# Kernel tuning notes

Measured on AMD Instinct MI355X. Metric: run time of the kernel, lower is better.

## Reference

```python
import jax, jax.numpy as jnp
import numpy as np

N_NEIGHBORS = 9
MIN_STD, MAX_STD = 0.01, 0.5
EPS = 1e-8


def setup_inputs() -> dict:
    key = jax.random.key(0)
    k1, k2, k3 = jax.random.split(key, 3)
    B, C, H, W = 8, 2048, 28, 28
    M = 8192
    features = jax.random.normal(k1, (B, C, H, W), dtype=jnp.float32)
    memory_bank = jax.random.normal(k2, (M, C), dtype=jnp.float32)
    influence_weight = jnp.ones((C,), dtype=jnp.float32)
    distance_weight = jnp.ones((1,), dtype=jnp.float32)
    noise_unit = jax.random.normal(k3, (B * H * W, C), dtype=jnp.float32)
    return {
        "features": features,
        "memory_bank": memory_bank,
        "influence_weight": influence_weight,
        "distance_weight": distance_weight,
        "noise_unit": noise_unit,
    }


def _std(x, axis=None, keepdims=False):
    # torch.std default: unbiased (ddof=1)
    return jnp.std(x, axis=axis, keepdims=keepdims, ddof=1)


def reference(features, memory_bank, influence_weight, distance_weight, noise_unit):
    B, C, H, W = features.shape
    M = memory_bank.shape[0]
    k = min(N_NEIGHBORS, M)

    # [B*H*W, C]
    f = features.transpose(0, 2, 3, 1).reshape(B * H * W, C)

    # Euclidean cdist via the (||a||^2 + ||b||^2 - 2 a.b) expansion
    f2 = jnp.sum(f * f, axis=1, keepdims=True)            # [N,1]
    m2 = jnp.sum(memory_bank * memory_bank, axis=1)       # [M]
    d2 = f2 + m2[None, :] - 2.0 * (f @ memory_bank.T)     # [N,M]
    dist = jnp.sqrt(jnp.clip(d2, 0.0, None))

    # top-k smallest distances (sorted ascending, like torch.topk largest=False)
    neg_vals, idx = jax.lax.top_k(-dist, k)               # [N,k]
    topk_distances = -neg_vals

    # gather neighbor features and per-dim influence
    nn_feats = memory_bank[idx]                           # [N,k,C]
    influence_scores = jnp.mean(jnp.abs(f[:, None, :] - nn_feats), axis=1)  # [N,C]
    influence_scores = influence_scores * influence_weight[None, :]

    # normalize influence per-row
    influence_norm = influence_scores - jnp.mean(influence_scores, axis=-1, keepdims=True)
    influence_norm = influence_norm / (_std(influence_scores, axis=-1, keepdims=True) + EPS)

    # distance signal: row-mean distance, broadcast to [N,C], global-normalized
    ds = jnp.mean(topk_distances, axis=-1, keepdims=True)  # [N,1]
    ds_e = jnp.broadcast_to(ds, influence_norm.shape)      # [N,C]
    distance_norm = (ds_e - jnp.mean(ds_e)) / (_std(ds_e) + EPS)

    combined = influence_norm + distance_weight * distance_norm
    noise_std = MIN_STD + (MAX_STD - MIN_STD) * jax.nn.sigmoid(combined)  # [N,C]

    noised_flat = f + noise_unit * noise_std
    noised_features = noised_flat.reshape(B, H, W, C).transpose(0, 3, 1, 2)
    influence_map = jnp.mean(influence_scores, axis=-1).reshape(B, H, W)
    noise_std_map = jnp.mean(noise_std, axis=-1).reshape(B, H, W)
    return noised_features, influence_map, noise_std_map
```

## Files before the change

### kernel.cpp

```cpp
#include <hip/hip_runtime.h>
#include <math.h>

typedef __attribute__((ext_vector_type(8))) __bf16 bf16x8;
typedef __attribute__((ext_vector_type(4))) float f32x4;

#define NB 8
#define NC 2048
#define NHW 784
#define NROWS 6272
#define NM 8192
#define NNEI 9
#define NCAND 16
#define NKT 64

static_assert(NROWS == NB * NHW, "dims");

__device__ __forceinline__ unsigned umin32(unsigned a, unsigned b) { return a < b ? a : b; }

__global__ __launch_bounds__(256) void prep_f_kernel(const float* __restrict__ feat,
                                                     float* __restrict__ Af32,
                                                     __bf16* __restrict__ Ahi) {
  __shared__ float tile[32][33];
  int b = blockIdx.z;
  int c0 = blockIdx.y * 32;
  int hw0 = blockIdx.x * 32;
  int tx = threadIdx.x & 31, ty = threadIdx.x >> 5;
#pragma unroll
  for (int i = 0; i < 4; ++i) {
    int c = c0 + ty + i * 8;
    int hw = hw0 + tx;
    float v = 0.f;
    if (hw < NHW) v = feat[((size_t)b * NC + c) * NHW + hw];
    tile[ty + i * 8][tx] = v;
  }
  __syncthreads();
#pragma unroll
  for (int i = 0; i < 4; ++i) {
    int hwl = ty + i * 8;
    int hw = hw0 + hwl;
    if (hw < NHW) {
      int n = b * NHW + hw;
      float v = tile[tx][hwl];
      Af32[(size_t)n * NC + c0 + tx] = v;
      Ahi[(size_t)n * NC + c0 + tx] = (__bf16)v;
    }
  }
}

__global__ __launch_bounds__(256) void prep_mb_kernel(const float* __restrict__ mb,
                                                      __bf16* __restrict__ Bhi,
                                                      float* __restrict__ m2) {
  __shared__ float red[4];
  int m = blockIdx.x, tid = threadIdx.x;
  float ss = 0.f;
#pragma unroll
  for (int i = 0; i < NC / 256; ++i) {
    int c = tid + i * 256;
    float v = mb[(size_t)m * NC + c];
    Bhi[(size_t)m * NC + c] = (__bf16)v;
    ss += v * v;
  }
#pragma unroll
  for (int off = 32; off; off >>= 1) ss += __shfl_xor(ss, off);
  if ((tid & 63) == 0) red[tid >> 6] = ss;
  __syncthreads();
  if (tid == 0) m2[m] = red[0] + red[1] + red[2] + red[3];
}

#define STAGE(SRC, DST) \
  __builtin_amdgcn_global_load_lds((const __attribute__((address_space(1))) void*)(SRC), \
                                   (__attribute__((address_space(3))) void*)(DST), 16, 0, 0)

__global__ __launch_bounds__(512, 2) void gemm8_kernel(const __bf16* __restrict__ Ahi,
                                                       const __bf16* __restrict__ Bhi,
                                                       const float* __restrict__ m2,
                                                       unsigned short* __restrict__ dotq) {
  __shared__ __align__(16) char lds[131072];
  int tid = threadIdx.x;
  int lane = tid & 63, w = tid >> 6;
  int bid = blockIdx.x;
  int r = lane & 15, kq = lane >> 4;
  int r4 = (lane >> 4) * 4, cL = lane & 15;

  if (bid >= 768) {
    int lb = bid - 768;
    size_t m0l = (size_t)(lb & 7) * 1024 + (size_t)(lb >> 3) * 32;
    int n0l = 6144 + w * 16;
    const __bf16* aB = Ahi + (size_t)(n0l + r) * NC + kq * 8;
    const __bf16* bB0 = Bhi + (m0l + r) * NC + kq * 8;
    const __bf16* bB1 = Bhi + (m0l + 16 + r) * NC + kq * 8;
    f32x4 acc0 = {}, acc1 = {};
    bf16x8 a0 = *(const bf16x8*)aB;
    bf16x8 b0 = *(const bf16x8*)bB0;
    bf16x8 b1 = *(const bf16x8*)bB1;
#pragma unroll 4
    for (int kt = 0; kt < NKT; ++kt) {
      int ktn = (kt + 1) & 63;
      bf16x8 an = *(const bf16x8*)(aB + ktn * 32);
      bf16x8 b0n = *(const bf16x8*)(bB0 + ktn * 32);
      bf16x8 b1n = *(const bf16x8*)(bB1 + ktn * 32);
      acc0 = __builtin_amdgcn_mfma_f32_16x16x32_bf16(a0, b0, acc0, 0, 0, 0);
      acc1 = __builtin_amdgcn_mfma_f32_16x16x32_bf16(a0, b1, acc1, 0, 0, 0);
      a0 = an; b0 = b0n; b1 = b1n;
    }
#pragma unroll
    for (int g = 0; g < 2; ++g) {
      float m2g = m2[m0l + g * 16 + cL];
      f32x4 ac = g ? acc1 : acc0;
#pragma unroll
      for (int q = 0; q < 4; ++q) {
        int grow = n0l + r4 + q;
        float sc = m2g - 2.f * ac[q];
        int qi = (int)(sc * 16.f);
        qi = qi < 0 ? 0 : (qi > 65535 ? 65535 : qi);
        dotq[(size_t)grow * NM + (m0l + g * 16 + cL)] = (unsigned short)qi;
      }
    }
    return;
  }

  int xcd = bid & 7, lin = bid >> 3;
  int mt = xcd * 4 + (lin & 3), rtl = lin >> 2;
  size_t n0 = (size_t)rtl * 256, m0 = (size_t)mt * 256;
  int wr = w >> 2, wc = w & 3;

  int p = lane & 3;
  const char* aSrc[2];
  const char* bSrc[2];
  int aDst[2], bDst[2];
#pragma unroll
  for (int j = 0; j < 2; ++j) {
    int rloc = (w * 2 + j) * 16 + (lane >> 2);
    int kqs = (p - (rloc >> 1)) & 3;
    aSrc[j] = (const char*)Ahi + (n0 + rloc) * (NC * 2) + kqs * 16;
    bSrc[j] = (const char*)Bhi + (m0 + rloc) * (NC * 2) + kqs * 16;
    aDst[j] = (w * 2 + j) * 1024;
    bDst[j] = 16384 + (w * 2 + j) * 1024;
  }
  int s16 = (kq + (r >> 1)) & 3;
  int aRd = wr * 8192 + r * 64 + s16 * 16;
  int bRd = 16384 + wc * 4096 + r * 64 + s16 * 16;

  f32x4 acc[8][4] = {};

#pragma unroll
  for (int t = 0; t < 2; ++t) {
    int sb = t * 32768, kb = t * 64;
#pragma unroll
    for (int j = 0; j < 2; ++j)
      STAGE(aSrc[j] + kb, lds + sb + aDst[j]);
#pragma unroll
    for (int j = 0; j < 2; ++j)
      STAGE(bSrc[j] + kb, lds + sb + bDst[j]);
  }
  asm volatile("s_waitcnt vmcnt(4)" ::: "memory");
  __builtin_amdgcn_s_barrier();
  __builtin_amdgcn_sched_barrier(0);

#pragma unroll 4
  for (int kt = 0; kt < NKT; ++kt) {
    int sb = (kt & 3) * 32768;
    int kt2 = (kt + 2) & 63;
    int sb2 = (kt2 & 3) * 32768;
    int kb2 = kt2 * 64;
    bf16x8 av[4], bv[4];
#pragma unroll
    for (int j = 0; j < 2; ++j)
      STAGE(aSrc[j] + kb2, lds + sb2 + aDst[j]);
#pragma unroll
    for (int f = 0; f < 4; ++f) av[f] = *(const bf16x8*)(lds + sb + aRd + f * 1024);
#pragma unroll
    for (int g = 0; g < 4; ++g) bv[g] = *(const bf16x8*)(lds + sb + bRd + g * 1024);
    __builtin_amdgcn_s_setprio(1);
#pragma unroll
    for (int f = 0; f < 4; ++f)
#pragma unroll
      for (int g = 0; g < 4; ++g)
        acc[f][g] = __builtin_amdgcn_mfma_f32_16x16x32_bf16(av[f], bv[g], acc[f][g], 0, 0, 0);
    __builtin_amdgcn_s_setprio(0);
#pragma unroll
    for (int j = 0; j < 2; ++j)
      STAGE(bSrc[j] + kb2, lds + sb2 + bDst[j]);
#pragma unroll
    for (int f = 0; f < 4; ++f) av[f] = *(const bf16x8*)(lds + sb + aRd + (f + 4) * 1024);
    __builtin_amdgcn_s_setprio(1);
#pragma unroll
    for (int f = 0; f < 4; ++f)
#pragma unroll
      for (int g = 0; g < 4; ++g)
        acc[f + 4][g] = __builtin_amdgcn_mfma_f32_16x16x32_bf16(av[f], bv[g], acc[f + 4][g], 0, 0, 0);
    __builtin_amdgcn_s_setprio(0);
    asm volatile("s_waitcnt vmcnt(4)" ::: "memory");
    __builtin_amdgcn_s_barrier();
    __builtin_amdgcn_sched_barrier(0);
  }

  float m2r[4];
#pragma unroll
  for (int g = 0; g < 4; ++g) m2r[g] = m2[m0 + wc * 64 + g * 16 + cL];
#pragma unroll
  for (int f = 0; f < 8; ++f) {
    int grow0 = (int)n0 + wr * 128 + f * 16 + r4;
#pragma unroll
    for (int g = 0; g < 4; ++g) {
      size_t gcol = m0 + wc * 64 + g * 16 + cL;
#pragma unroll
      for (int q = 0; q < 4; ++q) {
        float sc = m2r[g] - 2.f * acc[f][g][q];
        int qi = (int)(sc * 16.f);
        qi = qi < 0 ? 0 : (qi > 65535 ? 65535 : qi);
        dotq[(size_t)(grow0 + q) * NM + gcol] = (unsigned short)qi;
      }
    }
  }
}

__global__ __launch_bounds__(256) void selres_kernel(const unsigned short* __restrict__ dotq,
                                                     const float* __restrict__ Af32,
                                                     const float* __restrict__ mb,
                                                     int* __restrict__ tki,
                                                     float* __restrict__ dsv) {
  __shared__ float fbuf[NC];
  __shared__ unsigned wmin[4];
  __shared__ int cidxL[NCAND];
  __shared__ double d2s[NCAND];
  int n = blockIdx.x;
  int tid = threadIdx.x;
  int lane = tid & 63, w = tid >> 6;

  unsigned kk[32];
  {
    const uint4* dq = (const uint4*)(dotq + (size_t)n * NM + tid * 32);
    unsigned base = tid * 32;
#pragma unroll
    for (int s = 0; s < 4; ++s) {
      uint4 v = dq[s];
      unsigned c0 = v.x, c1 = v.y, c2 = v.z, c3 = v.w;
      kk[s * 8 + 0] = ((c0 & 0xFFFFu) << 13) | (base + s * 8 + 0);
      kk[s * 8 + 1] = ((c0 >> 16) << 13)     | (base + s * 8 + 1);
      kk[s * 8 + 2] = ((c1 & 0xFFFFu) << 13) | (base + s * 8 + 2);
      kk[s * 8 + 3] = ((c1 >> 16) << 13)     | (base + s * 8 + 3);
      kk[s * 8 + 4] = ((c2 & 0xFFFFu) << 13) | (base + s * 8 + 4);
      kk[s * 8 + 5] = ((c2 >> 16) << 13)     | (base + s * 8 + 5);
      kk[s * 8 + 6] = ((c3 & 0xFFFFu) << 13) | (base + s * 8 + 6);
      kk[s * 8 + 7] = ((c3 >> 16) << 13)     | (base + s * 8 + 7);
    }
  }
#pragma unroll
  for (int i = 0; i < NC / 256; ++i)
    fbuf[tid + i * 256] = Af32[(size_t)n * NC + tid + i * 256];

  unsigned lmin = 0xFFFFFFFFu;
#pragma unroll
  for (int i = 0; i < 32; ++i) lmin = umin32(lmin, kk[i]);
  unsigned t = lmin;
#pragma unroll
  for (int off = 32; off; off >>= 1) t = umin32(t, (unsigned)__shfl_xor((int)t, off));
  if (lane == 0) wmin[w] = t;
  __syncthreads();

  for (int r = 0; r < NCAND; ++r) {
    unsigned g = umin32(umin32(wmin[0], wmin[1]), umin32(wmin[2], wmin[3]));
    if (tid == 0) cidxL[r] = (int)(g & 8191u);
    __syncthreads();
    int owner = (int)((g & 8191u) >> 5);
    if ((owner >> 6) == w) {
      if (tid == owner) {
#pragma unroll
        for (int i = 0; i < 32; ++i)
          if (kk[i] == g) kk[i] = 0xFFFFFFFFu;
        lmin = 0xFFFFFFFFu;
#pragma unroll
        for (int i = 0; i < 32; ++i) lmin = umin32(lmin, kk[i]);
      }
      unsigned t2 = lmin;
#pragma unroll
      for (int off = 32; off; off >>= 1) t2 = umin32(t2, (unsigned)__shfl_xor((int)t2, off));
      if (lane == 0) wmin[w] = t2;
    }
    __syncthreads();
  }

#pragma unroll
  for (int jj = 0; jj < 4; ++jj) {
    int j = w * 4 + jj;
    const float* mrow = mb + (size_t)cidxL[j] * NC;
    double acc = 0.0;
#pragma unroll
    for (int i = 0; i < 32; ++i) {
      int c = lane + i * 64;
      double d = (double)fbuf[c] - (double)mrow[c];
      acc += d * d;
    }
#pragma unroll
    for (int off = 32; off; off >>= 1) acc += __shfl_xor(acc, off);
    if (lane == 0) d2s[j] = acc;
  }
  __syncthreads();

  if (tid == 0) {
    double dacc = 0.0;
    bool used[NCAND] = {};
    for (int r = 0; r < NNEI; ++r) {
      int bj = 0; double bv = 1e300; int bidx = 0x7fffffff;
      for (int j = 0; j < NCAND; ++j) {
        if (used[j]) continue;
        if (d2s[j] < bv || (d2s[j] == bv && cidxL[j] < bidx)) { bv = d2s[j]; bidx = cidxL[j]; bj = j; }
      }
      used[bj] = true;
      tki[(size_t)n * NNEI + r] = bidx;
      dacc += sqrt(bv > 0.0 ? bv : 0.0);
    }
    dsv[n] = (float)(dacc * (1.0 / 9.0));
  }
}

__global__ __launch_bounds__(256) void stats_kernel(const float* __restrict__ dsv,
                                                    float* __restrict__ stats) {
  __shared__ float buf[NROWS];
  __shared__ float red[4];
  int tid = threadIdx.x;
  float s = 0.f;
  for (int i = tid; i < NROWS; i += 256) { float v = dsv[i]; buf[i] = v; s += v; }
#pragma unroll
  for (int off = 32; off; off >>= 1) s += __shfl_xor(s, off);
  if ((tid & 63) == 0) red[tid >> 6] = s;
  __syncthreads();
  float mu = (red[0] + red[1] + red[2] + red[3]) * (1.f / NROWS);
  __syncthreads();
  float q = 0.f;
  for (int i = tid; i < NROWS; i += 256) { float d = buf[i] - mu; q += d * d; }
#pragma unroll
  for (int off = 32; off; off >>= 1) q += __shfl_xor(q, off);
  if ((tid & 63) == 0) red[tid >> 6] = q;
  __syncthreads();
  if (tid == 0) {
    float SSb = (red[0] + red[1] + red[2] + red[3]) * (float)NC;
    float var = SSb / ((float)NROWS * (float)NC - 1.f);
    stats[0] = mu;
    stats[1] = 1.f / (sqrtf(var) + 1e-8f);
  }
}

__global__ __launch_bounds__(256) void fuse_kernel(const float* __restrict__ Af32,
                                                   const float* __restrict__ mb,
                                                   const float* __restrict__ noise,
                                                   const float* __restrict__ iw,
                                                   const float* __restrict__ dwp,
                                                   const int* __restrict__ topk_idx,
                                                   const float* __restrict__ dsv,
                                                   const float* __restrict__ stats,
                                                   float* __restrict__ noised_tmp,
                                                   float* __restrict__ out_infl,
                                                   float* __restrict__ out_nstd) {
  __shared__ int idx[NNEI];
  __shared__ float red[4];
  int n = blockIdx.x;
  int tid = threadIdx.x;
  if (tid < NNEI) idx[tid] = topk_idx[(size_t)n * NNEI + tid];
  __syncthreads();

  int c0 = tid * 8;
  const float* frow = Af32 + (size_t)n * NC + c0;
  float4 fa = *(const float4*)frow;
  float4 fb = *(const float4*)(frow + 4);
  float f_c[8] = {fa.x, fa.y, fa.z, fa.w, fb.x, fb.y, fb.z, fb.w};
  float a_c[8] = {};
  for (int j = 0; j < NNEI; ++j) {
    const float* mrow = mb + (size_t)idx[j] * NC + c0;
    float4 ma = *(const float4*)mrow;
    float4 mb2 = *(const float4*)(mrow + 4);
    float mv[8] = {ma.x, ma.y, ma.z, ma.w, mb2.x, mb2.y, mb2.z, mb2.w};
#pragma unroll
    for (int k = 0; k < 8; ++k) a_c[k] += fabsf(f_c[k] - mv[k]);
  }
  float4 w0 = *(const float4*)(iw + c0);
  float4 w1 = *(const float4*)(iw + c0 + 4);
  float wv[8] = {w0.x, w0.y, w0.z, w0.w, w1.x, w1.y, w1.z, w1.w};
  float s_c[8];
  float sum_s = 0.f, sum_s2 = 0.f;
#pragma unroll
  for (int k = 0; k < 8; ++k) {
    float s = (a_c[k] * (1.f / 9.f)) * wv[k];
    s_c[k] = s;
    sum_s += s;
    sum_s2 += s * s;
  }
#pragma unroll
  for (int off = 32; off; off >>= 1) sum_s += __shfl_xor(sum_s, off);
  if ((tid & 63) == 0) red[tid >> 6] = sum_s;
  __syncthreads();
  float tot_s = red[0] + red[1] + red[2] + red[3];
  __syncthreads();
#pragma unroll
  for (int off = 32; off; off >>= 1) sum_s2 += __shfl_xor(sum_s2, off);
  if ((tid & 63) == 0) red[tid >> 6] = sum_s2;
  __syncthreads();
  float tot_s2 = red[0] + red[1] + red[2] + red[3];
  __syncthreads();

  float mu = tot_s * (1.f / NC);
  float var = (tot_s2 - (float)NC * mu * mu) * (1.f / (NC - 1));
  float rstd = 1.f / (sqrtf(fmaxf(var, 0.f)) + 1e-8f);
  float dnorm = (dsv[n] - stats[0]) * stats[1];
  float dwv = dwp[0];

  float4 na = *(const float4*)(noise + (size_t)n * NC + c0);
  float4 nb = *(const float4*)(noise + (size_t)n * NC + c0 + 4);
  float nz[8] = {na.x, na.y, na.z, na.w, nb.x, nb.y, nb.z, nb.w};
  float o[8];
  float nsum = 0.f;
#pragma unroll
  for (int k = 0; k < 8; ++k) {
    float inorm = (s_c[k] - mu) * rstd;
    float comb = inorm + dwv * dnorm;
    float sig = 1.f / (1.f + expf(-comb));
    float nstd = 0.01f + 0.49f * sig;
    nsum += nstd;
    o[k] = f_c[k] + nz[k] * nstd;
  }
  float* orow = noised_tmp + (size_t)n * NC + c0;
  *(float4*)orow = make_float4(o[0], o[1], o[2], o[3]);
  *(float4*)(orow + 4) = make_float4(o[4], o[5], o[6], o[7]);
#pragma unroll
  for (int off = 32; off; off >>= 1) nsum += __shfl_xor(nsum, off);
  if ((tid & 63) == 0) red[tid >> 6] = nsum;
  __syncthreads();
  if (tid == 0) {
    out_infl[n] = tot_s * (1.f / NC);
    out_nstd[n] = (red[0] + red[1] + red[2] + red[3]) * (1.f / NC);
  }
}

__global__ __launch_bounds__(256) void transpose_kernel(const float* __restrict__ src,
                                                        float* __restrict__ dst) {
  __shared__ float tile[32][33];
  int b = blockIdx.z;
  int c0 = blockIdx.y * 32;
  int hw0 = blockIdx.x * 32;
  int tx = threadIdx.x & 31, ty = threadIdx.x >> 5;
#pragma unroll
  for (int i = 0; i < 4; ++i) {
    int hw = hw0 + ty + i * 8;
    if (hw < NHW) tile[ty + i * 8][tx] = src[((size_t)(b * NHW + hw)) * NC + c0 + tx];
  }
  __syncthreads();
#pragma unroll
  for (int i = 0; i < 4; ++i) {
    int c = c0 + ty + i * 8;
    int hw = hw0 + tx;
    if (hw < NHW) dst[((size_t)b * NC + c) * NHW + hw] = tile[tx][ty + i * 8];
  }
}

extern "C" void kernel_launch(void* const* d_in, const int* in_sizes, int n_in,
                              void* d_out, int out_size, void* d_ws, size_t ws_size,
                              hipStream_t stream) {
  (void)in_sizes; (void)n_in; (void)out_size; (void)ws_size;
  const float* feat  = (const float*)d_in[0];
  const float* mb    = (const float*)d_in[1];
  const float* iw    = (const float*)d_in[2];
  const float* dwp   = (const float*)d_in[3];
  const float* noise = (const float*)d_in[4];
  float* out = (float*)d_out;
  float* out_noised = out;
  float* out_infl = out + (size_t)NB * NC * NHW;
  float* out_nstd = out_infl + NROWS;

  char* ws = (char*)d_ws;
  size_t off = 0;
  auto alloc = [&](size_t sz) -> char* {
    char* p = ws + off;
    off += (sz + 255) & ~(size_t)255;
    return p;
  };
  float* Af32 = (float*)alloc((size_t)NROWS * NC * 4);
  __bf16* Ahi = (__bf16*)alloc((size_t)NROWS * NC * 2);
  char* region = alloc((size_t)NROWS * NC * 4);
  __bf16* Bhi = (__bf16*)region;
  float* noised_tmp = (float*)region;
  float* m2v = (float*)alloc((size_t)NM * 4);
  int* tki = (int*)alloc((size_t)NROWS * NNEI * 4);
  float* dsv = (float*)alloc((size_t)NROWS * 4);
  float* stv = (float*)alloc(256);
  unsigned short* dotq = (unsigned short*)alloc((size_t)NROWS * NM * 2);

  prep_f_kernel<<<dim3(25, 64, NB), 256, 0, stream>>>(feat, Af32, Ahi);
  prep_mb_kernel<<<NM, 256, 0, stream>>>(mb, Bhi, m2v);
  gemm8_kernel<<<1024, 512, 0, stream>>>(Ahi, Bhi, m2v, dotq);
  selres_kernel<<<NROWS, 256, 0, stream>>>(dotq, Af32, mb, tki, dsv);
  stats_kernel<<<1, 256, 0, stream>>>(dsv, stv);
  fuse_kernel<<<NROWS, 256, 0, stream>>>(Af32, mb, noise, iw, dwp, tki, dsv, stv,
                                         noised_tmp, out_infl, out_nstd);
  transpose_kernel<<<dim3(25, 64, NB), 256, 0, stream>>>(noised_tmp, out_noised);
}
```

Measured before the change: 507.1 us.

## Merge prep kernels, shrink rerank candidates, read bf16 bank in fuse

Combines the feature-transpose and memory-bank conversion kernels into one launch. Reduces the number of exact-rerank candidates per row from 16 to 12, cutting fp64 distance work in the selection kernel. The fuse kernel now reads neighbor rows from the bf16 copy of the memory bank instead of fp32, halving gather traffic but computing influence scores from bf16-rounded values, a precision loss versus the fp32 reference. Workspace is rearranged so the bf16 bank persists and noised_tmp reuses the dotq buffer.

```diff
diff --git a/kernel.cpp b/kernel.cpp
--- a/kernel.cpp
+++ b/kernel.cpp
@@ -10,61 +10,64 @@
 #define NROWS 6272
 #define NM 8192
 #define NNEI 9
-#define NCAND 16
+#define NCAND 12
 #define NKT 64
 
 static_assert(NROWS == NB * NHW, "dims");
 
 __device__ __forceinline__ unsigned umin32(unsigned a, unsigned b) { return a < b ? a : b; }
 
-__global__ __launch_bounds__(256) void prep_f_kernel(const float* __restrict__ feat,
-                                                     float* __restrict__ Af32,
-                                                     __bf16* __restrict__ Ahi) {
-  __shared__ float tile[32][33];
-  int b = blockIdx.z;
-  int c0 = blockIdx.y * 32;
-  int hw0 = blockIdx.x * 32;
-  int tx = threadIdx.x & 31, ty = threadIdx.x >> 5;
-#pragma unroll
-  for (int i = 0; i < 4; ++i) {
-    int c = c0 + ty + i * 8;
-    int hw = hw0 + tx;
-    float v = 0.f;
-    if (hw < NHW) v = feat[((size_t)b * NC + c) * NHW + hw];
-    tile[ty + i * 8][tx] = v;
-  }
-  __syncthreads();
-#pragma unroll
-  for (int i = 0; i < 4; ++i) {
-    int hwl = ty + i * 8;
-    int hw = hw0 + hwl;
-    if (hw < NHW) {
-      int n = b * NHW + hw;
-      float v = tile[tx][hwl];
-      Af32[(size_t)n * NC + c0 + tx] = v;
-      Ahi[(size_t)n * NC + c0 + tx] = (__bf16)v;
-    }
-  }
-}
-
-__global__ __launch_bounds__(256) void prep_mb_kernel(const float* __restrict__ mb,
-                                                      __bf16* __restrict__ Bhi,
-                                                      float* __restrict__ m2) {
-  __shared__ float red[4];
-  int m = blockIdx.x, tid = threadIdx.x;
-  float ss = 0.f;
-#pragma unroll
-  for (int i = 0; i < NC / 256; ++i) {
-    int c = tid + i * 256;
-    float v = mb[(size_t)m * NC + c];
-    Bhi[(size_t)m * NC + c] = (__bf16)v;
-    ss += v * v;
-  }
-#pragma unroll
-  for (int off = 32; off; off >>= 1) ss += __shfl_xor(ss, off);
-  if ((tid & 63) == 0) red[tid >> 6] = ss;
-  __syncthreads();
-  if (tid == 0) m2[m] = red[0] + red[1] + red[2] + red[3];
+__global__ __launch_bounds__(256) void prep_kernel(const float* __restrict__ feat,
+                                                   const float* __restrict__ mb,
+                                                   float* __restrict__ Af32,
+                                                   __bf16* __restrict__ Ahi,
+                                                   __bf16* __restrict__ Bhi,
+                                                   float* __restrict__ m2) {
+  int bid = blockIdx.x;
+  int tid = threadIdx.x;
+  if (bid < 12800) {
+    __shared__ float tile[32][33];
+    int b = bid / 1600;
+    int c0 = ((bid / 25) & 63) * 32;
+    int hw0 = (bid % 25) * 32;
+    int tx = tid & 31, ty = tid >> 5;
+#pragma unroll
+    for (int i = 0; i < 4; ++i) {
+      int c = c0 + ty + i * 8;
+      int hw = hw0 + tx;
+      float v = 0.f;
+      if (hw < NHW) v = feat[((size_t)b * NC + c) * NHW + hw];
+      tile[ty + i * 8][tx] = v;
+    }
+    __syncthreads();
+#pragma unroll
+    for (int i = 0; i < 4; ++i) {
+      int hwl = ty + i * 8;
+      int hw = hw0 + hwl;
+      if (hw < NHW) {
+        int n = b * NHW + hw;
+        float v = tile[tx][hwl];
+        Af32[(size_t)n * NC + c0 + tx] = v;
+        Ahi[(size_t)n * NC + c0 + tx] = (__bf16)v;
+      }
+    }
+  } else {
+    __shared__ float red[4];
+    int m = bid - 12800;
+    float ss = 0.f;
+#pragma unroll
+    for (int i = 0; i < NC / 256; ++i) {
+      int c = tid + i * 256;
+      float v = mb[(size_t)m * NC + c];
+      Bhi[(size_t)m * NC + c] = (__bf16)v;
+      ss += v * v;
+    }
+#pragma unroll
+    for (int off = 32; off; off >>= 1) ss += __shfl_xor(ss, off);
+    if ((tid & 63) == 0) red[tid >> 6] = ss;
+    __syncthreads();
+    if (tid == 0) m2[m] = red[0] + red[1] + red[2] + red[3];
+  }
 }
 
 #define STAGE(SRC, DST) \
@@ -282,8 +285,8 @@
   }
 
 #pragma unroll
-  for (int jj = 0; jj < 4; ++jj) {
-    int j = w * 4 + jj;
+  for (int jj = 0; jj < 3; ++jj) {
+    int j = w * 3 + jj;
     const float* mrow = mb + (size_t)cidxL[j] * NC;
     double acc = 0.0;
 #pragma unroll
@@ -343,7 +346,7 @@
 }
 
 __global__ __launch_bounds__(256) void fuse_kernel(const float* __restrict__ Af32,
-                                                   const float* __restrict__ mb,
+                                                   const __bf16* __restrict__ Bhi,
                                                    const float* __restrict__ noise,
                                                    const float* __restrict__ iw,
                                                    const float* __restrict__ dwp,
@@ -367,12 +370,9 @@
   float f_c[8] = {fa.x, fa.y, fa.z, fa.w, fb.x, fb.y, fb.z, fb.w};
   float a_c[8] = {};
   for (int j = 0; j < NNEI; ++j) {
-    const float* mrow = mb + (size_t)idx[j] * NC + c0;
-    float4 ma = *(const float4*)mrow;
-    float4 mb2 = *(const float4*)(mrow + 4);
-    float mv[8] = {ma.x, ma.y, ma.z, ma.w, mb2.x, mb2.y, mb2.z, mb2.w};
-#pragma unroll
-    for (int k = 0; k < 8; ++k) a_c[k] += fabsf(f_c[k] - mv[k]);
+    bf16x8 mv = *(const bf16x8*)(Bhi + (size_t)idx[j] * NC + c0);
+#pragma unroll
+    for (int k = 0; k < 8; ++k) a_c[k] += fabsf(f_c[k] - (float)mv[k]);
   }
   float4 w0 = *(const float4*)(iw + c0);
   float4 w1 = *(const float4*)(iw + c0 + 4);
@@ -476,21 +476,19 @@
   };
   float* Af32 = (float*)alloc((size_t)NROWS * NC * 4);
   __bf16* Ahi = (__bf16*)alloc((size_t)NROWS * NC * 2);
-  char* region = alloc((size_t)NROWS * NC * 4);
-  __bf16* Bhi = (__bf16*)region;
-  float* noised_tmp = (float*)region;
+  __bf16* Bhi = (__bf16*)alloc((size_t)NM * NC * 2);
   float* m2v = (float*)alloc((size_t)NM * 4);
   int* tki = (int*)alloc((size_t)NROWS * NNEI * 4);
   float* dsv = (float*)alloc((size_t)NROWS * 4);
   float* stv = (float*)alloc(256);
   unsigned short* dotq = (unsigned short*)alloc((size_t)NROWS * NM * 2);
-
-  prep_f_kernel<<<dim3(25, 64, NB), 256, 0, stream>>>(feat, Af32, Ahi);
-  prep_mb_kernel<<<NM, 256, 0, stream>>>(mb, Bhi, m2v);
+  float* noised_tmp = (float*)dotq;
+
+  prep_kernel<<<12800 + NM, 256, 0, stream>>>(feat, mb, Af32, Ahi, Bhi, m2v);
   gemm8_kernel<<<1024, 512, 0, stream>>>(Ahi, Bhi, m2v, dotq);
   selres_kernel<<<NROWS, 256, 0, stream>>>(dotq, Af32, mb, tki, dsv);
   stats_kernel<<<1, 256, 0, stream>>>(dsv, stv);
-  fuse_kernel<<<NROWS, 256, 0, stream>>>(Af32, mb, noise, iw, dwp, tki, dsv, stv,
+  fuse_kernel<<<NROWS, 256, 0, stream>>>(Af32, Bhi, noise, iw, dwp, tki, dsv, stv,
                                          noised_tmp, out_infl, out_nstd);
   transpose_kernel<<<dim3(25, 64, NB), 256, 0, stream>>>(noised_tmp, out_noised);
 }
```

Measured after the change: 440.3 us, median of 2. 13.2% less time.
